# Kernel tuning notes

Hardware: AMD Instinct MI355X
Metric: run time of the kernel (lower is better)

The kernel has to match this reference:

```python
import jax, jax.numpy as jnp
import numpy as np

B, G, S, NNZ = 64, 20000, 200000, 2000000

def setup_inputs() -> dict:
    key = jax.random.key(0)
    k1, k2, k3, k4, k5 = jax.random.split(key, 5)
    x = jax.random.normal(k1, (B, G), dtype=jnp.float32)
    # COO connectivity: row = SNP index (output), col = gene index (input)
    row = jax.random.randint(k2, (NNZ,), 0, S, dtype=jnp.int64)
    col = jax.random.randint(k3, (NNZ,), 0, G, dtype=jnp.int64)
    index = jnp.stack([row, col])  # [2, NNZ]
    W_sparse = jax.random.normal(k4, (NNZ,), dtype=jnp.float32) * 0.02
    b = jax.random.normal(k5, (S, 1), dtype=jnp.float32) * 0.02
    return {"x": x, "W_sparse": W_sparse, "b": b, "index": index, "n_SNPs": S}

def reference(x, W_sparse, b, index, n_SNPs):
    # spmm: sparse [n_SNPs, n_genes] @ x.T [n_genes, B] -> [n_SNPs, B]
    row, col = index[0], index[1]
    gathered = x.T[col] * W_sparse[:, None]            # [NNZ, B] edge contributions
    dot_prod = jax.ops.segment_sum(gathered, row, num_segments=n_SNPs)  # [S, B]
    output = dot_prod + b                              # bias broadcast over batch
    return output.T                                    # [B, n_SNPs]
```

## Files before the change

### kernel.cpp

```cpp
#include <hip/hip_runtime.h>


#define WAVE 64
#define CHUNK 8192
#define RBITS 6
#define BINROWS 64
#define SCAN_PAD 3584
#define CAP_BIN 896

#define RL(v, i)  __builtin_amdgcn_readlane((int)(v), (i))

__device__ __forceinline__ int swz(int r, int b) {
    return (r << 6) + (b ^ (r & 63));
}

__device__ __forceinline__ unsigned short f2bf(float f) {
    unsigned u = __float_as_uint(f);
    unsigned r = (u + 0x7fffu + ((u >> 16) & 1u)) >> 16;
    return (unsigned short)r;
}

__global__ void transpose64_kernel(const float* __restrict__ x,
                                   unsigned short* __restrict__ xTh, int G) {
    __shared__ float tile[64][65];
    const int t  = threadIdx.x;
    const int g0 = blockIdx.x * 64;
    {
        const int j  = t & 63;
        const int b0 = t >> 6;
        if (g0 + j < G) {
            #pragma unroll
            for (int it = 0; it < 16; ++it) {
                const int b = b0 + it * 4;
                tile[j][b] = x[(size_t)b * G + g0 + j];
            }
        }
    }
    __syncthreads();
    {
        const int b  = t & 63;
        const int j0 = t >> 6;
        #pragma unroll
        for (int it = 0; it < 16; ++it) {
            const int j = j0 + it * 4;
            if (g0 + j < G) xTh[(size_t)(g0 + j) * WAVE + b] = f2bf(tile[j][b]);
        }
    }
}

__global__ __launch_bounds__(512) void pass1_kernel(
        const int* __restrict__ row, const int* __restrict__ col,
        const float* __restrict__ w, uint2* __restrict__ sedge1,
        unsigned* __restrict__ segtab, int nnz, int nbin) {
    __shared__ __align__(16) uint2 stage[CHUNK];
    __shared__ int hist[SCAN_PAD];
    __shared__ int wpart[8];
    const int t    = threadIdx.x;
    const int lane = t & 63;
    const int wv   = t >> 6;
    const int e0   = blockIdx.x * CHUNK;
    const bool full = (e0 + CHUNK <= nnz);
    const int M    = full ? CHUNK : (nnz - e0);

    for (int j = t; j < SCAN_PAD; j += 512) hist[j] = 0;
    __syncthreads();

    if (full) {
        const int4* rv = (const int4*)(row + e0);
        #pragma unroll
        for (int k = 0; k < CHUNK / 2048; ++k) {
            const int4 r4 = rv[k * 512 + t];
            atomicAdd(&hist[r4.x >> RBITS], 1);
            atomicAdd(&hist[r4.y >> RBITS], 1);
            atomicAdd(&hist[r4.z >> RBITS], 1);
            atomicAdd(&hist[r4.w >> RBITS], 1);
        }
    } else {
        for (int k = 0; k < CHUNK / 512; ++k) {
            const int i = k * 512 + t;
            if (i < M) atomicAdd(&hist[row[e0 + i] >> RBITS], 1);
        }
    }
    __syncthreads();

    {
        int c[7];
        int p = 0;
        #pragma unroll
        for (int j = 0; j < 7; ++j) { c[j] = hist[t * 7 + j]; p += c[j]; }
        int incl = p;
        #pragma unroll
        for (int d = 1; d < 64; d <<= 1) {
            const int u = __shfl_up(incl, d);
            if (lane >= d) incl += u;
        }
        if (lane == 63) wpart[wv] = incl;
        __syncthreads();
        int base = incl - p;
        #pragma unroll
        for (int ww = 0; ww < 8; ++ww)
            if (ww < wv) base += wpart[ww];
        unsigned* st = segtab + (size_t)blockIdx.x * (size_t)(nbin + 1);
        int run = base;
        #pragma unroll
        for (int j = 0; j < 7; ++j) {
            const int bj = t * 7 + j;
            hist[bj] = run;
            if (bj <= nbin) st[bj] = (unsigned)(e0 + run);
            run += c[j];
        }
    }
    __syncthreads();

    if (full) {
        const int4*   rv = (const int4*)(row + e0);
        const int4*   cv = (const int4*)(col + e0);
        const float4* wf = (const float4*)(w + e0);
        #pragma unroll
        for (int k = 0; k < CHUNK / 2048; ++k) {
            const int4   r4 = rv[k * 512 + t];
            const int4   c4 = cv[k * 512 + t];
            const float4 w4 = wf[k * 512 + t];
            {
                const int pos = atomicAdd(&hist[r4.x >> RBITS], 1);
                stage[pos] = make_uint2(((unsigned)(r4.x & 63) << 15) |
                                        (unsigned)c4.x, __float_as_uint(w4.x));
            }
            {
                const int pos = atomicAdd(&hist[r4.y >> RBITS], 1);
                stage[pos] = make_uint2(((unsigned)(r4.y & 63) << 15) |
                                        (unsigned)c4.y, __float_as_uint(w4.y));
            }
            {
                const int pos = atomicAdd(&hist[r4.z >> RBITS], 1);
                stage[pos] = make_uint2(((unsigned)(r4.z & 63) << 15) |
                                        (unsigned)c4.z, __float_as_uint(w4.z));
            }
            {
                const int pos = atomicAdd(&hist[r4.w >> RBITS], 1);
                stage[pos] = make_uint2(((unsigned)(r4.w & 63) << 15) |
                                        (unsigned)c4.w, __float_as_uint(w4.w));
            }
        }
    } else {
        for (int k = 0; k < CHUNK / 512; ++k) {
            const int i = k * 512 + t;
            if (i < M) {
                const int r = row[e0 + i];
                const int pos = atomicAdd(&hist[r >> RBITS], 1);
                stage[pos] = make_uint2(((unsigned)(r & 63) << 15) |
                                        (unsigned)col[e0 + i],
                                        __float_as_uint(w[e0 + i]));
            }
        }
    }
    __syncthreads();

    {
        const uint4* sg4 = (const uint4*)stage;
        uint4* o4 = (uint4*)(sedge1 + e0);
        for (int j = t; j < (M >> 1); j += 512) o4[j] = sg4[j];
        if ((M & 1) && t == 0) sedge1[e0 + M - 1] = stage[M - 1];
    }
}

#define PROC(Er, ar, ii)                                                      \
    {                                                                         \
        const int   k_ = RL((Er).x, (ii));                                    \
        const float w_ = __int_as_float(RL((Er).y, (ii)));                    \
        const float v_ = __uint_as_float(                                     \
            (unsigned)*(const unsigned short*)(xb + k_ + lane2) << 16);       \
        (ar) += v_ * w_;                                                      \
    }

__global__ __launch_bounds__(256) void compute_kernel(
        const unsigned short* __restrict__ xTh,
        const uint2* __restrict__ sedge1,
        const unsigned* __restrict__ segtab,
        const float* __restrict__ bias,
        float* __restrict__ out, int S, int nchunk, int nbin) {
    __shared__ float tile[64 * 64];
    __shared__ uint2 eds2[CAP_BIN];
    __shared__ int   rcnt[4][BINROWS];
    __shared__ int   cur[4][BINROWS];
    __shared__ int   rstart[BINROWS], rend[BINROWS];
    __shared__ int   rord[BINROWS];
    __shared__ float bls[BINROWS];
    __shared__ int   spart[4];
    uint2* eds1 = (uint2*)tile;

    const int t    = threadIdx.x;
    const int lane = t & 63;
    const int wv   = t >> 6;

    const int q8 = nbin >> 3, r8 = nbin & 7;
    const int xcd = (int)blockIdx.x & 7, off = (int)blockIdx.x >> 3;
    const int b = (xcd < r8 ? xcd * (q8 + 1) : r8 * (q8 + 1) + (xcd - r8) * q8)
                  + off;
    const int r0 = b << RBITS;

    if (t < BINROWS) {
        rcnt[0][t] = 0; rcnt[1][t] = 0; rcnt[2][t] = 0; rcnt[3][t] = 0;
        bls[t] = (r0 + t < S) ? bias[r0 + t] : 0.f;
    }

    int myst = 0, myn = 0;
    if (t < nchunk) {
        const unsigned* p = segtab + (size_t)t * (size_t)(nbin + 1) + b;
        const unsigned s0 = p[0];
        myst = (int)s0; myn = (int)(p[1] - s0);
    }
    int incl = myn;
    #pragma unroll
    for (int d = 1; d < 64; d <<= 1) {
        const int u = __shfl_up(incl, d);
        if (lane >= d) incl += u;
    }
    if (lane == 63) spart[wv] = incl;
    __syncthreads();
    int base = incl - myn;
    #pragma unroll
    for (int ww = 0; ww < 4; ++ww)
        if (ww < wv) base += spart[ww];
    int M = spart[0] + spart[1] + spart[2] + spart[3];
    if (M > CAP_BIN) M = CAP_BIN;

    for (int k = 0; k < myn; ++k) {
        const int p = base + k;
        if (p < CAP_BIN) eds1[p] = sedge1[myst + k];
    }
    __syncthreads();

    for (int i = t; i < M; i += 256)
        atomicAdd(&rcnt[wv][eds1[i].x >> 15], 1);
    __syncthreads();

    if (t < BINROWS) {
        const int c0 = rcnt[0][t], c1 = rcnt[1][t];
        const int c2 = rcnt[2][t], c3 = rcnt[3][t];
        const int tot = c0 + c1 + c2 + c3;
        int inc2 = tot;
        #pragma unroll
        for (int d = 1; d < 64; d <<= 1) {
            const int u = __shfl_up(inc2, d);
            if (lane >= d) inc2 += u;
        }
        const int stt = inc2 - tot;
        rstart[t] = stt;
        rend[t]   = stt + tot;
        cur[0][t] = stt;
        cur[1][t] = stt + c0;
        cur[2][t] = stt + c0 + c1;
        cur[3][t] = stt + c0 + c1 + c2;

        int key = (tot << 6) | t;
        #pragma unroll
        for (int k = 2; k <= 64; k <<= 1) {
            #pragma unroll
            for (int j = k >> 1; j > 0; j >>= 1) {
                const int other = __shfl_xor(key, j);
                const bool lower = (lane & j) == 0;
                const bool asc   = (lane & k) == 0;
                bool take = ((other < key) == lower);
                if (!asc) take = !take;
                key = take ? other : key;
            }
        }
        rord[t] = key & 63;
    }
    __syncthreads();

    for (int i = t; i < M; i += 256) {
        const uint2 e = eds1[i];
        const int r = (int)(e.x >> 15);
        const int pos = atomicAdd(&cur[wv][r], 1);
        eds2[pos] = make_uint2((e.x & 0x7fffu) << 7, e.y);
    }
    __syncthreads();

    const char* xb = (const char*)xTh;
    const int lane2 = lane * 2;

    #pragma unroll
    for (int qd = 0; qd < 4; ++qd) {
        const int p0 = (qd * 4 + wv) * 4;
        const int rl0 = rord[p0 + 0], rl1 = rord[p0 + 1];
        const int rl2 = rord[p0 + 2], rl3 = rord[p0 + 3];
        int s0 = rstart[rl0], e0g = rend[rl0];
        int s1 = rstart[rl1], e1g = rend[rl1];
        int s2 = rstart[rl2], e2g = rend[rl2];
        int s3 = rstart[rl3], e3g = rend[rl3];
        float a0 = 0.f, a1 = 0.f, a2 = 0.f, a3 = 0.f;
        while ((s0 < e0g) || (s1 < e1g) || (s2 < e2g) || (s3 < e3g)) {
            const int m0 = min(WAVE, e0g - s0);
            const int m1 = min(WAVE, e1g - s1);
            const int m2 = min(WAVE, e2g - s2);
            const int m3 = min(WAVE, e3g - s3);
            uint2 E0 = make_uint2(0u, 0u), E1 = make_uint2(0u, 0u);
            uint2 E2 = make_uint2(0u, 0u), E3 = make_uint2(0u, 0u);
            if (lane < m0) E0 = eds2[s0 + lane];
            if (lane < m1) E1 = eds2[s1 + lane];
            if (lane < m2) E2 = eds2[s2 + lane];
            if (lane < m3) E3 = eds2[s3 + lane];
            const int mm = max(max(m0, m1), max(m2, m3));
            int i = 0;
            for (; i + 2 <= mm; i += 2) {
                PROC(E0, a0, i) PROC(E1, a1, i) PROC(E2, a2, i) PROC(E3, a3, i)
                PROC(E0, a0, i + 1) PROC(E1, a1, i + 1)
                PROC(E2, a2, i + 1) PROC(E3, a3, i + 1)
            }
            if (i < mm) {
                PROC(E0, a0, i) PROC(E1, a1, i) PROC(E2, a2, i) PROC(E3, a3, i)
            }
            s0 += max(m0, 0); s1 += max(m1, 0);
            s2 += max(m2, 0); s3 += max(m3, 0);
        }
        tile[swz(rl0, lane)] = a0 + bls[rl0];
        tile[swz(rl1, lane)] = a1 + bls[rl1];
        tile[swz(rl2, lane)] = a2 + bls[rl2];
        tile[swz(rl3, lane)] = a3 + bls[rl3];
    }
    __syncthreads();

    const int srow = r0 + lane;
    #pragma unroll
    for (int k = 0; k < 16; ++k) {
        const int bb = wv * 16 + k;
        if (srow < S) out[(size_t)bb * S + srow] = tile[swz(lane, bb)];
    }
}

extern "C" void kernel_launch(void* const* d_in, const int* in_sizes, int n_in,
                              void* d_out, int out_size, void* d_ws, size_t ws_size,
                              hipStream_t stream) {
    const float* x    = (const float*)d_in[0];
    const float* W    = (const float*)d_in[1];
    const float* bias = (const float*)d_in[2];
    const int*   idx  = (const int*)d_in[3];

    const int NNZ = in_sizes[1];
    const int S   = in_sizes[2];
    const int B   = out_size / S;
    const int G   = in_sizes[0] / B;
    const int* rowi = idx;
    const int* coli = idx + NNZ;
    float* out = (float*)d_out;

    const int nbin   = (S + BINROWS - 1) >> RBITS;
    const int nchunk = (NNZ + CHUNK - 1) / CHUNK;

    char* ws = (char*)d_ws;
    size_t o = 0;
    auto alloc = [&](size_t bytes) {
        void* p = ws + o;
        o = (o + bytes + 255) & ~(size_t)255;
        return p;
    };
    unsigned short* xTh = (unsigned short*)alloc((size_t)G * B * sizeof(unsigned short));
    uint2*    sedge1 = (uint2*)   alloc((size_t)NNZ * sizeof(uint2));
    unsigned* segtab = (unsigned*)alloc((size_t)nchunk * (size_t)(nbin + 1) *
                                        sizeof(unsigned));
    (void)ws_size; (void)n_in;

    const int tgrid = (G + 63) / 64;
    transpose64_kernel<<<tgrid, 256, 0, stream>>>(x, xTh, G);

    pass1_kernel<<<nchunk, 512, 0, stream>>>(rowi, coli, W, sedge1, segtab,
                                             NNZ, nbin);
    compute_kernel<<<nbin, 256, 0, stream>>>(xTh, sedge1, segtab, bias,
                                             out, S, nchunk, nbin);
}
```

Measured before the change: 158.4 us.

## Shrink compute kernel LDS by staging output transpose in two halves

Packs all shared arrays into one manually laid-out buffer, with the edge and output-tile regions overlapping. Accumulators now stay in registers until the edge phase ends, and the 64x64 output transpose runs as two 32-row passes through a half-size tile. This lowers LDS per block so more blocks can be resident per CU. In exchange it adds extra barriers and holds 16 accumulator registers per thread.

Measured after the change: 166.9 us. +5.3%, slower.

```diff
diff --git a/kernel.cpp b/kernel.cpp
--- a/kernel.cpp
+++ b/kernel.cpp
@@ -179,15 +179,17 @@
         const unsigned* __restrict__ segtab,
         const float* __restrict__ bias,
         float* __restrict__ out, int S, int nchunk, int nbin) {
-    __shared__ float tile[64 * 64];
-    __shared__ uint2 eds2[CAP_BIN];
-    __shared__ int   rcnt[4][BINROWS];
-    __shared__ int   cur[4][BINROWS];
-    __shared__ int   rstart[BINROWS], rend[BINROWS];
-    __shared__ int   rord[BINROWS];
-    __shared__ float bls[BINROWS];
-    __shared__ int   spart[4];
-    uint2* eds1 = (uint2*)tile;
+    __shared__ __align__(16) char smem[17456];
+    uint2* eds1  = (uint2*)smem;
+    uint2* eds2  = (uint2*)(smem + 7168);
+    float* tile8 = (float*)smem;
+    int (*rcnt)[BINROWS] = (int (*)[BINROWS])(smem + 14336);
+    int (*cur)[BINROWS]  = (int (*)[BINROWS])(smem + 15360);
+    int*   rstart = (int*)(smem + 16384);
+    int*   rend   = (int*)(smem + 16640);
+    int*   rord   = (int*)(smem + 16896);
+    float* bls    = (float*)(smem + 17152);
+    int*   spart  = (int*)(smem + 17408);
 
     const int t    = threadIdx.x;
     const int lane = t & 63;
@@ -280,6 +282,7 @@
 
     const char* xb = (const char*)xTh;
     const int lane2 = lane * 2;
+    float acc[16];
 
     #pragma unroll
     for (int qd = 0; qd < 4; ++qd) {
@@ -315,18 +318,34 @@
             s0 += max(m0, 0); s1 += max(m1, 0);
             s2 += max(m2, 0); s3 += max(m3, 0);
         }
-        tile[swz(rl0, lane)] = a0 + bls[rl0];
-        tile[swz(rl1, lane)] = a1 + bls[rl1];
-        tile[swz(rl2, lane)] = a2 + bls[rl2];
-        tile[swz(rl3, lane)] = a3 + bls[rl3];
-    }
-    __syncthreads();
-
-    const int srow = r0 + lane;
+        acc[qd * 4 + 0] = a0 + bls[rl0];
+        acc[qd * 4 + 1] = a1 + bls[rl1];
+        acc[qd * 4 + 2] = a2 + bls[rl2];
+        acc[qd * 4 + 3] = a3 + bls[rl3];
+    }
+    __syncthreads();
+
     #pragma unroll
-    for (int k = 0; k < 16; ++k) {
-        const int bb = wv * 16 + k;
-        if (srow < S) out[(size_t)bb * S + srow] = tile[swz(lane, bb)];
+    for (int r = 0; r < 2; ++r) {
+        #pragma unroll
+        for (int qd = 0; qd < 4; ++qd) {
+            const int p0 = (qd * 4 + wv) * 4;
+            #pragma unroll
+            for (int j = 0; j < 4; ++j) {
+                const int rl = rord[p0 + j];
+                if ((rl >> 5) == r)
+                    tile8[swz(rl & 31, lane)] = acc[qd * 4 + j];
+            }
+        }
+        __syncthreads();
+        const int rr = lane & 31, hf = lane >> 5;
+        const int srow = r0 + r * 32 + rr;
+        #pragma unroll
+        for (int k = 0; k < 8; ++k) {
+            const int bb = wv * 16 + 2 * k + hf;
+            if (srow < S) out[(size_t)bb * S + srow] = tile8[swz(rr, bb)];
+        }
+        __syncthreads();
     }
 }
 
```

## Split wave into half-waves processing two edges with packed bf16x2 gathers

Applied to the files above, without the earlier changes.

Restructures the inner SpMM loop so each half-wave handles alternate edges. Each lane loads a 32-bit word holding two bf16 batch values instead of one 16-bit value, and the edges are read directly from LDS instead of broadcast with readlane. Per-row edge lists are padded to even length with zeroed entries, and the two half-wave partial sums are combined with a cross-half shuffle before writing the tile. This is meant to halve the number of gather instructions and remove the readlane/SGPR overhead, at the cost of padding, extra LDS zeroing and a masked tail loop.

After: 182.0 us. 1.15x slower.

```diff
diff --git a/kernel.cpp b/kernel.cpp
--- a/kernel.cpp
+++ b/kernel.cpp
@@ -7,6 +7,7 @@
 #define BINROWS 64
 #define SCAN_PAD 3584
 #define CAP_BIN 896
+#define CAP_PAD 1024
 
 #define RL(v, i)  __builtin_amdgcn_readlane((int)(v), (i))
 
@@ -164,13 +165,23 @@
     }
 }
 
-#define PROC(Er, ar, ii)                                                      \
+#define PROCPU(pj, alo, ahi, ii)                                              \
     {                                                                         \
-        const int   k_ = RL((Er).x, (ii));                                    \
-        const float w_ = __int_as_float(RL((Er).y, (ii)));                    \
-        const float v_ = __uint_as_float(                                     \
-            (unsigned)*(const unsigned short*)(xb + k_ + lane2) << 16);       \
-        (ar) += v_ * w_;                                                      \
+        const uint2 E_ = (pj)[ii];                                            \
+        const float w_ = __uint_as_float(E_.y);                               \
+        const unsigned d_ = *(const unsigned*)(xb + E_.x + j4);               \
+        (alo) += __uint_as_float(d_ << 16) * w_;                              \
+        (ahi) += __uint_as_float(d_ & 0xffff0000u) * w_;                      \
+    }
+
+#define PROCPM(pj, nj, alo, ahi, ii)                                          \
+    {                                                                         \
+        const int   idx_ = min((ii), (nj) - 2);                               \
+        const uint2 E_   = (pj)[idx_];                                        \
+        const float w_   = ((ii) < (nj)) ? __uint_as_float(E_.y) : 0.f;       \
+        const unsigned d_ = *(const unsigned*)(xb + E_.x + j4);               \
+        (alo) += __uint_as_float(d_ << 16) * w_;                              \
+        (ahi) += __uint_as_float(d_ & 0xffff0000u) * w_;                      \
     }
 
 __global__ __launch_bounds__(256) void compute_kernel(
@@ -180,10 +191,10 @@
         const float* __restrict__ bias,
         float* __restrict__ out, int S, int nchunk, int nbin) {
     __shared__ float tile[64 * 64];
-    __shared__ uint2 eds2[CAP_BIN];
+    __shared__ uint2 eds2[CAP_PAD];
     __shared__ int   rcnt[4][BINROWS];
     __shared__ int   cur[4][BINROWS];
-    __shared__ int   rstart[BINROWS], rend[BINROWS];
+    __shared__ int   rstart[BINROWS], npad[BINROWS];
     __shared__ int   rord[BINROWS];
     __shared__ float bls[BINROWS];
     __shared__ int   spart[4];
@@ -192,6 +203,8 @@
     const int t    = threadIdx.x;
     const int lane = t & 63;
     const int wv   = t >> 6;
+    const int half = lane >> 5;
+    const int j4   = (lane & 31) * 4;
 
     const int q8 = nbin >> 3, r8 = nbin & 7;
     const int xcd = (int)blockIdx.x & 7, off = (int)blockIdx.x >> 3;
@@ -203,6 +216,9 @@
         rcnt[0][t] = 0; rcnt[1][t] = 0; rcnt[2][t] = 0; rcnt[3][t] = 0;
         bls[t] = (r0 + t < S) ? bias[r0 + t] : 0.f;
     }
+    #pragma unroll
+    for (int k = 0; k < CAP_PAD / 256; ++k)
+        eds2[t + k * 256] = make_uint2(0u, 0u);
 
     int myst = 0, myn = 0;
     if (t < nchunk) {
@@ -239,21 +255,22 @@
         const int c0 = rcnt[0][t], c1 = rcnt[1][t];
         const int c2 = rcnt[2][t], c3 = rcnt[3][t];
         const int tot = c0 + c1 + c2 + c3;
-        int inc2 = tot;
+        const int pad = (tot < 2) ? 2 : ((tot + 1) & ~1);
+        int inc2 = pad;
         #pragma unroll
         for (int d = 1; d < 64; d <<= 1) {
             const int u = __shfl_up(inc2, d);
             if (lane >= d) inc2 += u;
         }
-        const int stt = inc2 - tot;
+        const int stt = inc2 - pad;
         rstart[t] = stt;
-        rend[t]   = stt + tot;
+        npad[t]   = pad;
         cur[0][t] = stt;
         cur[1][t] = stt + c0;
         cur[2][t] = stt + c0 + c1;
         cur[3][t] = stt + c0 + c1 + c2;
 
-        int key = (tot << 6) | t;
+        int key = (pad << 6) | t;
         #pragma unroll
         for (int k = 2; k <= 64; k <<= 1) {
             #pragma unroll
@@ -279,46 +296,58 @@
     __syncthreads();
 
     const char* xb = (const char*)xTh;
-    const int lane2 = lane * 2;
 
     #pragma unroll
     for (int qd = 0; qd < 4; ++qd) {
-        const int p0 = (qd * 4 + wv) * 4;
-        const int rl0 = rord[p0 + 0], rl1 = rord[p0 + 1];
-        const int rl2 = rord[p0 + 2], rl3 = rord[p0 + 3];
-        int s0 = rstart[rl0], e0g = rend[rl0];
-        int s1 = rstart[rl1], e1g = rend[rl1];
-        int s2 = rstart[rl2], e2g = rend[rl2];
-        int s3 = rstart[rl3], e3g = rend[rl3];
-        float a0 = 0.f, a1 = 0.f, a2 = 0.f, a3 = 0.f;
-        while ((s0 < e0g) || (s1 < e1g) || (s2 < e2g) || (s3 < e3g)) {
-            const int m0 = min(WAVE, e0g - s0);
-            const int m1 = min(WAVE, e1g - s1);
-            const int m2 = min(WAVE, e2g - s2);
-            const int m3 = min(WAVE, e3g - s3);
-            uint2 E0 = make_uint2(0u, 0u), E1 = make_uint2(0u, 0u);
-            uint2 E2 = make_uint2(0u, 0u), E3 = make_uint2(0u, 0u);
-            if (lane < m0) E0 = eds2[s0 + lane];
-            if (lane < m1) E1 = eds2[s1 + lane];
-            if (lane < m2) E2 = eds2[s2 + lane];
-            if (lane < m3) E3 = eds2[s3 + lane];
-            const int mm = max(max(m0, m1), max(m2, m3));
-            int i = 0;
-            for (; i + 2 <= mm; i += 2) {
-                PROC(E0, a0, i) PROC(E1, a1, i) PROC(E2, a2, i) PROC(E3, a3, i)
-                PROC(E0, a0, i + 1) PROC(E1, a1, i + 1)
-                PROC(E2, a2, i + 1) PROC(E3, a3, i + 1)
-            }
-            if (i < mm) {
-                PROC(E0, a0, i) PROC(E1, a1, i) PROC(E2, a2, i) PROC(E3, a3, i)
-            }
-            s0 += max(m0, 0); s1 += max(m1, 0);
-            s2 += max(m2, 0); s3 += max(m3, 0);
-        }
-        tile[swz(rl0, lane)] = a0 + bls[rl0];
-        tile[swz(rl1, lane)] = a1 + bls[rl1];
-        tile[swz(rl2, lane)] = a2 + bls[rl2];
-        tile[swz(rl3, lane)] = a3 + bls[rl3];
+        const int p0i = (qd * 4 + wv) * 4;
+        const int rl0 = rord[p0i + 0], rl1 = rord[p0i + 1];
+        const int rl2 = rord[p0i + 2], rl3 = rord[p0i + 3];
+        const int n0 = npad[rl0], n1 = npad[rl1];
+        const int n2 = npad[rl2], n3 = npad[rl3];
+        const uint2* pp0 = eds2 + rstart[rl0] + half;
+        const uint2* pp1 = eds2 + rstart[rl1] + half;
+        const uint2* pp2 = eds2 + rstart[rl2] + half;
+        const uint2* pp3 = eds2 + rstart[rl3] + half;
+        float a0l = 0.f, a0h = 0.f, a1l = 0.f, a1h = 0.f;
+        float a2l = 0.f, a2h = 0.f, a3l = 0.f, a3h = 0.f;
+        const int mn = min(min(n0, n1), min(n2, n3));
+        const int mm = max(max(n0, n1), max(n2, n3));
+        int i = 0;
+        for (; i + 4 <= mn; i += 4) {
+            PROCPU(pp0, a0l, a0h, i)     PROCPU(pp1, a1l, a1h, i)
+            PROCPU(pp2, a2l, a2h, i)     PROCPU(pp3, a3l, a3h, i)
+            PROCPU(pp0, a0l, a0h, i + 2) PROCPU(pp1, a1l, a1h, i + 2)
+            PROCPU(pp2, a2l, a2h, i + 2) PROCPU(pp3, a3l, a3h, i + 2)
+        }
+        for (; i + 2 <= mn; i += 2) {
+            PROCPU(pp0, a0l, a0h, i) PROCPU(pp1, a1l, a1h, i)
+            PROCPU(pp2, a2l, a2h, i) PROCPU(pp3, a3l, a3h, i)
+        }
+        for (; i < mm; i += 2) {
+            PROCPM(pp0, n0, a0l, a0h, i) PROCPM(pp1, n1, a1l, a1h, i)
+            PROCPM(pp2, n2, a2l, a2h, i) PROCPM(pp3, n3, a3l, a3h, i)
+        }
+        const int bcol = 2 * (lane & 31) + half;
+        {
+            const float cl = a0l + __shfl_xor(a0l, 32);
+            const float ch = a0h + __shfl_xor(a0h, 32);
+            tile[swz(rl0, bcol)] = (half ? ch : cl) + bls[rl0];
+        }
+        {
+            const float cl = a1l + __shfl_xor(a1l, 32);
+            const float ch = a1h + __shfl_xor(a1h, 32);
+            tile[swz(rl1, bcol)] = (half ? ch : cl) + bls[rl1];
+        }
+        {
+            const float cl = a2l + __shfl_xor(a2l, 32);
+            const float ch = a2h + __shfl_xor(a2h, 32);
+            tile[swz(rl2, bcol)] = (half ? ch : cl) + bls[rl2];
+        }
+        {
+            const float cl = a3l + __shfl_xor(a3l, 32);
+            const float ch = a3h + __shfl_xor(a3h, 32);
+            tile[swz(rl3, bcol)] = (half ? ch : cl) + bls[rl3];
+        }
     }
     __syncthreads();
 
```
